# Kernel tuning notes

Measured on AMD Instinct MI355X. Metric: run time of the kernel, lower is better.

The kernel has to match this reference:

```python
import jax, jax.numpy as jnp
import numpy as np

N_TX = 1_000_000   # transaction nodes
N_W  = 250_000     # wallet nodes
E    = 2_000_000   # edges per relation
F_TX, F_W = 64, 32 # raw feature dims
H, OUT = 64, 2     # hidden, out (module defaults)


def setup_inputs() -> dict:
    key = jax.random.key(0)
    ks = jax.random.split(key, 40)
    f32 = jnp.float32
    def w(i, shape):
        return jax.random.normal(ks[i], shape, dtype=f32) * 0.05
    inp = {}
    inp["x_tx"] = jax.random.normal(ks[0], (N_TX, F_TX), dtype=f32)
    inp["x_w"]  = jax.random.normal(ks[1], (N_W, F_W), dtype=f32)
    inp["src_tw"] = jax.random.randint(ks[2], (E,), 0, N_TX)
    inp["dst_tw"] = jax.random.randint(ks[3], (E,), 0, N_W)
    inp["src_wt"] = jax.random.randint(ks[4], (E,), 0, N_W)
    inp["dst_wt"] = jax.random.randint(ks[5], (E,), 0, N_TX)
    # lin_in per node type
    inp["Win_tx"], inp["bin_tx"] = w(6, (F_TX, H)), w(7, (H,))
    inp["Win_w"],  inp["bin_w"]  = w(8, (F_W, H)),  w(9, (H,))
    # conv1: SAGEConv per edge type (lin_l has bias, lin_r no bias)
    inp["Wl1_tw"], inp["bl1_tw"], inp["Wr1_tw"] = w(10, (H, H)), w(11, (H,)), w(12, (H, H))
    inp["Wl1_wt"], inp["bl1_wt"], inp["Wr1_wt"] = w(13, (H, H)), w(14, (H,)), w(15, (H, H))
    # conv2
    inp["Wl2_tw"], inp["bl2_tw"], inp["Wr2_tw"] = w(16, (H, H)), w(17, (H,)), w(18, (H, H))
    inp["Wl2_wt"], inp["bl2_wt"], inp["Wr2_wt"] = w(19, (H, H)), w(20, (H,)), w(21, (H, H))
    # tx head
    inp["Wh1"], inp["bh1"] = w(22, (H, H)), w(23, (H,))
    inp["Wh2"], inp["bh2"] = w(24, (H, OUT)), w(25, (OUT,))
    return inp


def _sage(x_src, x_dst, src, dst, Wl, bl, Wr, n_dst):
    # PyG SAGEConv: lin_l(mean_{j->i} x_src[j]) + lin_r(x_dst[i])
    agg = jax.ops.segment_sum(x_src[src], dst, num_segments=n_dst)
    cnt = jax.ops.segment_sum(jnp.ones((src.shape[0],), x_src.dtype), dst,
                              num_segments=n_dst)
    mean = agg / jnp.maximum(cnt, 1.0)[:, None]
    return mean @ Wl + bl + x_dst @ Wr


def reference(x_tx, x_w, src_tw, dst_tw, src_wt, dst_wt,
              Win_tx, bin_tx, Win_w, bin_w,
              Wl1_tw, bl1_tw, Wr1_tw, Wl1_wt, bl1_wt, Wr1_wt,
              Wl2_tw, bl2_tw, Wr2_tw, Wl2_wt, bl2_wt, Wr2_wt,
              Wh1, bh1, Wh2, bh2):
    # per-type input projection
    h_tx = x_tx @ Win_tx + bin_tx   # [N_TX, H]
    h_w  = x_w @ Win_w + bin_w      # [N_W, H]
    # conv1 (HeteroConv aggr='sum'; each dst type has one relation) + relu
    w1 = jax.nn.relu(_sage(h_tx, h_w,  src_tw, dst_tw, Wl1_tw, bl1_tw, Wr1_tw, N_W))
    t1 = jax.nn.relu(_sage(h_w,  h_tx, src_wt, dst_wt, Wl1_wt, bl1_wt, Wr1_wt, N_TX))
    # conv2 + relu
    w2 = jax.nn.relu(_sage(t1, w1, src_tw, dst_tw, Wl2_tw, bl2_tw, Wr2_tw, N_W))
    t2 = jax.nn.relu(_sage(w1, t1, src_wt, dst_wt, Wl2_wt, bl2_wt, Wr2_wt, N_TX))
    # tx head (dropout inactive in eval)
    logits = jax.nn.relu(t2 @ Wh1 + bh1) @ Wh2 + bh2  # [N_TX, 2]
    return (logits, t2, w2)
```

## Files before the change

### kernel.cpp

```cpp
#include <hip/hip_runtime.h>
#include <hip/hip_bf16.h>

typedef __hip_bfloat16 bf16;
typedef __attribute__((ext_vector_type(8))) short bf16x8;
typedef __attribute__((ext_vector_type(4))) float f32x4;

__device__ __forceinline__ float b2f(bf16 v) { return __bfloat162float(v); }
__device__ __forceinline__ bf16 f2b(float v) { return __float2bfloat16(v); }
__device__ __forceinline__ unsigned short f2bb(float v) {
    unsigned int u = __float_as_uint(v);
    u += 0x7fffu + ((u >> 16) & 1u);
    return (unsigned short)(u >> 16);
}
__device__ __forceinline__ float b2fx(bf16x8 v, int k) {
    return __uint_as_float(((unsigned int)(unsigned short)v[k]) << 16);
}

__device__ __forceinline__ f32x4 mfma16(bf16x8 a, bf16x8 b, f32x4 c) {
    return __builtin_amdgcn_mfma_f32_16x16x32_bf16(a, b, c, 0, 0, 0);
}

__device__ __forceinline__ bf16x8 load_bfrag(const float* __restrict__ W, int k0, int col) {
    bf16x8 f;
#pragma unroll
    for (int j = 0; j < 8; ++j)
        f[j] = (short)f2bb(W[(size_t)(k0 + j) * 64 + col]);
    return f;
}

__device__ __forceinline__ int swzH(int row, int b) {
    return row * 128 + (b ^ ((row & 7) << 4));
}

__global__ void count_rank2_kernel(const int* __restrict__ dst_tw, int* __restrict__ deg_w,
                                   int* __restrict__ rank_tw, int ne_tw,
                                   const int* __restrict__ dst_wt, int* __restrict__ deg_tx,
                                   int* __restrict__ rank_wt, int ne_wt) {
    int e = blockIdx.x * 256 + threadIdx.x;
    if (e < ne_tw) rank_tw[e] = atomicAdd(&deg_w[dst_tw[e]], 1);
    else {
        int e2 = e - ne_tw;
        if (e2 < ne_wt) rank_wt[e2] = atomicAdd(&deg_tx[dst_wt[e2]], 1);
    }
}

__global__ void scan1m_kernel(const int* __restrict__ dw, int* __restrict__ ew,
                              int* __restrict__ pw, int nw, int npw,
                              const int* __restrict__ dt, int* __restrict__ et,
                              int* __restrict__ pt, int nt) {
    __shared__ int sT[256];
    const int* deg; int* excl; int* partial; int n; int b;
    if ((int)blockIdx.x < npw) { deg = dw; excl = ew; partial = pw; n = nw; b = blockIdx.x; }
    else { deg = dt; excl = et; partial = pt; n = nt; b = blockIdx.x - npw; }
    int tid = threadIdx.x;
    int base = b * 1024 + tid * 4;
    int v0 = (base + 0 < n) ? deg[base + 0] : 0;
    int v1 = (base + 1 < n) ? deg[base + 1] : 0;
    int v2 = (base + 2 < n) ? deg[base + 2] : 0;
    int v3 = (base + 3 < n) ? deg[base + 3] : 0;
    int t = v0 + v1 + v2 + v3;
    sT[tid] = t;
    __syncthreads();
    for (int off = 1; off < 256; off <<= 1) {
        int x = (tid >= off) ? sT[tid - off] : 0;
        __syncthreads();
        sT[tid] += x;
        __syncthreads();
    }
    int et2 = sT[tid] - t;
    if (tid == 255) partial[b] = sT[255];
    if (base + 0 < n) excl[base + 0] = et2;
    if (base + 1 < n) excl[base + 1] = et2 + v0;
    if (base + 2 < n) excl[base + 2] = et2 + v0 + v1;
    if (base + 3 < n) excl[base + 3] = et2 + v0 + v1 + v2;
}

__global__ void scan2m_kernel(int* __restrict__ pw, int npw, int* __restrict__ pt, int npt) {
    __shared__ int sT[256];
    __shared__ int carry;
    int* partial = blockIdx.x ? pt : pw;
    int np = blockIdx.x ? npt : npw;
    int tid = threadIdx.x;
    if (tid == 0) carry = 0;
    __syncthreads();
    for (int c = 0; c < np; c += 256) {
        int i = c + tid;
        int v = (i < np) ? partial[i] : 0;
        sT[tid] = v;
        __syncthreads();
        for (int off = 1; off < 256; off <<= 1) {
            int x = (tid >= off) ? sT[tid - off] : 0;
            __syncthreads();
            sT[tid] += x;
            __syncthreads();
        }
        int incl = sT[tid];
        int total = sT[255];
        if (i < np) partial[i] = carry + incl - v;
        __syncthreads();
        if (tid == 0) carry += total;
        __syncthreads();
    }
}

__global__ void scan3m_kernel(const int* __restrict__ ew, const int* __restrict__ pw,
                              int* __restrict__ rw, int nw, int nbw,
                              const int* __restrict__ et, const int* __restrict__ pt,
                              int* __restrict__ rt, int nt) {
    int b = blockIdx.x;
    const int* excl; const int* partial; int* rp; int n; int i;
    if (b < nbw) { i = b * 256 + threadIdx.x; excl = ew; partial = pw; rp = rw; n = nw; }
    else { i = (b - nbw) * 256 + threadIdx.x; excl = et; partial = pt; rp = rt; n = nt; }
    if (i < n) rp[i] = excl[i] + partial[i >> 10];
}

__device__ __forceinline__ void proj64_body(const float* __restrict__ x,
                                            const float* __restrict__ W,
                                            const float* __restrict__ b,
                                            bf16* __restrict__ out, int n, int bid) {
    int tid = threadIdx.x;
    int lane = tid & 63, w = tid >> 6;
    int lm = lane & 15, lq = lane >> 4;

    bf16x8 wc[4][2];
    float bv[4];
#pragma unroll
    for (int ct = 0; ct < 4; ++ct) {
        int colc = ct * 16 + lm;
        wc[ct][0] = load_bfrag(W, lq * 8, colc);
        wc[ct][1] = load_bfrag(W, 32 + lq * 8, colc);
        bv[ct] = b[colc];
    }

    int larow = w * 16 + lm;
    int row0 = bid * 512;
    if (row0 >= n) return;
    int ar = row0 + larow; ar = (ar < n) ? ar : (n - 1);
    const float* xrow = x + ((size_t)ar << 6);
    float4 p0 = *(const float4*)(xrow + lq * 8);
    float4 p1 = *(const float4*)(xrow + lq * 8 + 4);
    float4 p2 = *(const float4*)(xrow + 32 + lq * 8);
    float4 p3 = *(const float4*)(xrow + 32 + lq * 8 + 4);

    for (int g = 0; g < 8; ++g) {
        int gr0 = row0 + g * 64;
        if (gr0 >= n) break;
        float4 q0 = p0, q1 = p1, q2 = p2, q3 = p3;
        if (g < 7) {
            int nr = gr0 + 64 + larow; nr = (nr < n) ? nr : (n - 1);
            const float* nx = x + ((size_t)nr << 6);
            q0 = *(const float4*)(nx + lq * 8);
            q1 = *(const float4*)(nx + lq * 8 + 4);
            q2 = *(const float4*)(nx + 32 + lq * 8);
            q3 = *(const float4*)(nx + 32 + lq * 8 + 4);
        }
        bf16x8 a0, a1;
        a0[0] = (short)f2bb(p0.x); a0[1] = (short)f2bb(p0.y);
        a0[2] = (short)f2bb(p0.z); a0[3] = (short)f2bb(p0.w);
        a0[4] = (short)f2bb(p1.x); a0[5] = (short)f2bb(p1.y);
        a0[6] = (short)f2bb(p1.z); a0[7] = (short)f2bb(p1.w);
        a1[0] = (short)f2bb(p2.x); a1[1] = (short)f2bb(p2.y);
        a1[2] = (short)f2bb(p2.z); a1[3] = (short)f2bb(p2.w);
        a1[4] = (short)f2bb(p3.x); a1[5] = (short)f2bb(p3.y);
        a1[6] = (short)f2bb(p3.z); a1[7] = (short)f2bb(p3.w);
#pragma unroll
        for (int ct = 0; ct < 4; ++ct) {
            f32x4 acc = {0.f, 0.f, 0.f, 0.f};
            acc = mfma16(a0, wc[ct][0], acc);
            acc = mfma16(a1, wc[ct][1], acc);
            int colc = ct * 16 + lm;
#pragma unroll
            for (int r = 0; r < 4; ++r) {
                int grow = gr0 + w * 16 + lq * 4 + r;
                if (grow < n)
                    out[(size_t)grow * 64 + colc] = f2b(acc[r] + bv[ct]);
            }
        }
        p0 = q0; p1 = q1; p2 = q2; p3 = q3;
    }
}

__device__ __forceinline__ void proj32_body(const float* __restrict__ x,
                                            const float* __restrict__ W,
                                            const float* __restrict__ b,
                                            bf16* __restrict__ out, int n, int bid,
                                            float (*sW)[64], float* sb, float (*sx)[32]) {
    const int F = 32;
    int tid = threadIdx.x;
    for (int idx = tid; idx < F * 16; idx += 256)
        ((float4*)sW)[idx] = ((const float4*)W)[idx];
    if (tid < 64) sb[tid] = b[tid];
    int base = bid * 64;
    int w = tid >> 6, j = tid & 63;
    int lw = w * 4;
    for (int g = 0; g < 4; ++g) {
        int row0 = base + g * 16;
        __syncthreads();
        for (int idx = tid; idx < 4 * F; idx += 256) {
            int rr = idx / (F / 4), c4 = idx - rr * (F / 4);
            int row = row0 + rr;
            float4 v = (row < n) ? ((const float4*)x)[(size_t)row * (F / 4) + c4]
                                 : make_float4(0.f, 0.f, 0.f, 0.f);
            *(float4*)&sx[rr][c4 * 4] = v;
        }
        __syncthreads();
        float a0 = sb[j], a1 = sb[j], a2 = sb[j], a3 = sb[j];
#pragma unroll 2
        for (int k = 0; k < F; k += 4) {
            float w0 = sW[k][j], w1 = sW[k + 1][j], w2 = sW[k + 2][j], w3 = sW[k + 3][j];
            float4 m0 = *(const float4*)&sx[lw + 0][k];
            float4 m1 = *(const float4*)&sx[lw + 1][k];
            float4 m2 = *(const float4*)&sx[lw + 2][k];
            float4 m3 = *(const float4*)&sx[lw + 3][k];
            a0 += m0.x * w0 + m0.y * w1 + m0.z * w2 + m0.w * w3;
            a1 += m1.x * w0 + m1.y * w1 + m1.z * w2 + m1.w * w3;
            a2 += m2.x * w0 + m2.y * w1 + m2.z * w2 + m2.w * w3;
            a3 += m3.x * w0 + m3.y * w1 + m3.z * w2 + m3.w * w3;
        }
        int r0 = row0 + lw;
        if (r0 + 0 < n) out[(size_t)(r0 + 0) * 64 + j] = f2b(a0);
        if (r0 + 1 < n) out[(size_t)(r0 + 1) * 64 + j] = f2b(a1);
        if (r0 + 2 < n) out[(size_t)(r0 + 2) * 64 + j] = f2b(a2);
        if (r0 + 3 < n) out[(size_t)(r0 + 3) * 64 + j] = f2b(a3);
    }
}

__global__ __launch_bounds__(256)
void fused_front_kernel(const int* __restrict__ src_tw, const int* __restrict__ dst_tw,
                        const int* __restrict__ rank_tw, const int* __restrict__ rp_w,
                        int* __restrict__ col_tw, int ne_tw,
                        const int* __restrict__ src_wt, const int* __restrict__ dst_wt,
                        const int* __restrict__ rank_wt, const int* __restrict__ rp_tx,
                        int* __restrict__ col_wt, int ne_wt, int gsc,
                        const float* __restrict__ x_tx, const float* __restrict__ Win_tx,
                        const float* __restrict__ bin_tx, bf16* __restrict__ A, int n_tx, int gp64,
                        const float* __restrict__ x_w, const float* __restrict__ Win_w,
                        const float* __restrict__ bin_w, bf16* __restrict__ B, int n_w) {
    __shared__ float sW32[32][64];
    __shared__ float sb32[64];
    __shared__ float sx32[16][32];
    int bid = blockIdx.x;
    if (bid < gsc) {
        int e = bid * 256 + threadIdx.x;
        if (e < ne_tw) {
            col_tw[rp_w[dst_tw[e]] + rank_tw[e]] = src_tw[e];
        } else {
            int e2 = e - ne_tw;
            if (e2 < ne_wt)
                col_wt[rp_tx[dst_wt[e2]] + rank_wt[e2]] = src_wt[e2];
        }
    } else if (bid < gsc + gp64) {
        proj64_body(x_tx, Win_tx, bin_tx, A, n_tx, bid - gsc);
    } else {
        proj32_body(x_w, Win_w, bin_w, B, n_w, bid - gsc - gp64, sW32, sb32, sx32);
    }
}

#define GM_ACC(x, w) \
    a0 += (w) * b2fx(x, 0); a1 += (w) * b2fx(x, 1); \
    a2 += (w) * b2fx(x, 2); a3 += (w) * b2fx(x, 3); \
    a4 += (w) * b2fx(x, 4); a5 += (w) * b2fx(x, 5); \
    a6 += (w) * b2fx(x, 6); a7 += (w) * b2fx(x, 7);

__device__ __forceinline__ void gather_body(const bf16* __restrict__ h,
                                            const int* __restrict__ rowptr,
                                            const int* __restrict__ deg,
                                            const int* __restrict__ col,
                                            bf16* __restrict__ mean, int n, int bid) {
    int tid = threadIdx.x;
    int row = bid * 32 + (tid >> 3);
    if (row >= n) return;
    int fg = tid & 7;
    int base = rowptr[row];
    int d = deg[row];
    int lasto = (d > 0) ? d - 1 : 0;
    float a0 = 0.f, a1 = 0.f, a2 = 0.f, a3 = 0.f;
    float a4 = 0.f, a5 = 0.f, a6 = 0.f, a7 = 0.f;
    for (int e0 = 0; e0 < d; e0 += 8) {
        int o1 = (e0 + 1 < d) ? e0 + 1 : lasto;
        int o2 = (e0 + 2 < d) ? e0 + 2 : lasto;
        int o3 = (e0 + 3 < d) ? e0 + 3 : lasto;
        int o4 = (e0 + 4 < d) ? e0 + 4 : lasto;
        int o5 = (e0 + 5 < d) ? e0 + 5 : lasto;
        int o6 = (e0 + 6 < d) ? e0 + 6 : lasto;
        int o7 = (e0 + 7 < d) ? e0 + 7 : lasto;
        int s0 = col[base + e0], s1 = col[base + o1];
        int s2 = col[base + o2], s3 = col[base + o3];
        int s4 = col[base + o4], s5 = col[base + o5];
        int s6 = col[base + o6], s7 = col[base + o7];
        bf16x8 x0 = *(const bf16x8*)(h + ((size_t)s0 << 6) + (fg << 3));
        bf16x8 x1 = *(const bf16x8*)(h + ((size_t)s1 << 6) + (fg << 3));
        bf16x8 x2 = *(const bf16x8*)(h + ((size_t)s2 << 6) + (fg << 3));
        bf16x8 x3 = *(const bf16x8*)(h + ((size_t)s3 << 6) + (fg << 3));
        bf16x8 x4 = *(const bf16x8*)(h + ((size_t)s4 << 6) + (fg << 3));
        bf16x8 x5 = *(const bf16x8*)(h + ((size_t)s5 << 6) + (fg << 3));
        bf16x8 x6 = *(const bf16x8*)(h + ((size_t)s6 << 6) + (fg << 3));
        bf16x8 x7 = *(const bf16x8*)(h + ((size_t)s7 << 6) + (fg << 3));
        float w1 = (e0 + 1 < d) ? 1.f : 0.f;
        float w2 = (e0 + 2 < d) ? 1.f : 0.f;
        float w3 = (e0 + 3 < d) ? 1.f : 0.f;
        float w4 = (e0 + 4 < d) ? 1.f : 0.f;
        float w5 = (e0 + 5 < d) ? 1.f : 0.f;
        float w6 = (e0 + 6 < d) ? 1.f : 0.f;
        float w7 = (e0 + 7 < d) ? 1.f : 0.f;
        GM_ACC(x0, 1.f)
        GM_ACC(x1, w1)
        GM_ACC(x2, w2)
        GM_ACC(x3, w3)
        GM_ACC(x4, w4)
        GM_ACC(x5, w5)
        GM_ACC(x6, w6)
        GM_ACC(x7, w7)
    }
    float dd = fmaxf((float)d, 1.f);
    bf16x8 o;
    o[0] = (short)f2bb(a0 / dd); o[1] = (short)f2bb(a1 / dd);
    o[2] = (short)f2bb(a2 / dd); o[3] = (short)f2bb(a3 / dd);
    o[4] = (short)f2bb(a4 / dd); o[5] = (short)f2bb(a5 / dd);
    o[6] = (short)f2bb(a6 / dd); o[7] = (short)f2bb(a7 / dd);
    *(bf16x8*)(mean + ((size_t)row << 6) + (fg << 3)) = o;
}

__global__ __launch_bounds__(256)
void gather2_kernel(const bf16* __restrict__ hw, const int* __restrict__ rpw,
                    const int* __restrict__ dw, const int* __restrict__ cw,
                    bf16* __restrict__ mw, int nw, int gbw,
                    const bf16* __restrict__ ht, const int* __restrict__ rpt,
                    const int* __restrict__ dt, const int* __restrict__ ct,
                    bf16* __restrict__ mt, int nt) {
    if ((int)blockIdx.x < gbw) gather_body(hw, rpw, dw, cw, mw, nw, blockIdx.x);
    else                       gather_body(ht, rpt, dt, ct, mt, nt, blockIdx.x - gbw);
}

template<bool HEAD>
__device__ __forceinline__ void sage_body(
        const bf16* __restrict__ mean, const bf16* __restrict__ xd,
        const float* __restrict__ Wl, const float* __restrict__ bl,
        const float* __restrict__ Wr,
        float* __restrict__ outf, bf16* __restrict__ outb,
        const float* __restrict__ Wh1, const float* __restrict__ bh1,
        const float* __restrict__ Wh2, const float* __restrict__ bh2,
        float* __restrict__ logits, int n, int bid, short* sH) {
    int tid = threadIdx.x;
    int lane = tid & 63, w = tid >> 6;
    int lm = lane & 15, lq = lane >> 4;

    bf16x8 wc[4][4];
    bf16x8 wh[4][2];
    float blv[4], h1v[4], w2a[4], w2b[4];
#pragma unroll
    for (int ct = 0; ct < 4; ++ct) {
        int colc = ct * 16 + lm;
        wc[ct][0] = load_bfrag(Wl, lq * 8, colc);
        wc[ct][1] = load_bfrag(Wl, 32 + lq * 8, colc);
        wc[ct][2] = load_bfrag(Wr, lq * 8, colc);
        wc[ct][3] = load_bfrag(Wr, 32 + lq * 8, colc);
        blv[ct] = bl[colc];
        if (HEAD) {
            wh[ct][0] = load_bfrag(Wh1, lq * 8, colc);
            wh[ct][1] = load_bfrag(Wh1, 32 + lq * 8, colc);
            h1v[ct] = bh1[colc];
            w2a[ct] = Wh2[colc * 2 + 0];
            w2b[ct] = Wh2[colc * 2 + 1];
        }
    }
    float b20 = 0.f, b21 = 0.f;
    if (HEAD) { b20 = bh2[0]; b21 = bh2[1]; }

    int larow = w * 16 + lm;
    int row0 = bid * 512;
    if (row0 >= n) return;
    int ar = row0 + larow; ar = (ar < n) ? ar : (n - 1);
    const bf16* mrow = mean + ((size_t)ar << 6);
    const bf16* xrow = xd + ((size_t)ar << 6);
    bf16x8 a0 = *(const bf16x8*)(mrow + lq * 8);
    bf16x8 a1 = *(const bf16x8*)(mrow + 32 + lq * 8);
    bf16x8 a2 = *(const bf16x8*)(xrow + lq * 8);
    bf16x8 a3 = *(const bf16x8*)(xrow + 32 + lq * 8);

    for (int g = 0; g < 8; ++g) {
        int gr0 = row0 + g * 64;
        if (gr0 >= n) break;
        bf16x8 n0 = a0, n1 = a1, n2 = a2, n3 = a3;
        if (g < 7) {
            int nr = gr0 + 64 + larow; nr = (nr < n) ? nr : (n - 1);
            const bf16* nm = mean + ((size_t)nr << 6);
            const bf16* nx = xd + ((size_t)nr << 6);
            n0 = *(const bf16x8*)(nm + lq * 8);
            n1 = *(const bf16x8*)(nm + 32 + lq * 8);
            n2 = *(const bf16x8*)(nx + lq * 8);
            n3 = *(const bf16x8*)(nx + 32 + lq * 8);
        }
#pragma unroll
        for (int ct = 0; ct < 4; ++ct) {
            f32x4 acc = {0.f, 0.f, 0.f, 0.f};
            acc = mfma16(a0, wc[ct][0], acc);
            acc = mfma16(a1, wc[ct][1], acc);
            acc = mfma16(a2, wc[ct][2], acc);
            acc = mfma16(a3, wc[ct][3], acc);
            int colc = ct * 16 + lm;
#pragma unroll
            for (int r = 0; r < 4; ++r) {
                int lrow = w * 16 + lq * 4 + r;
                int grow = gr0 + lrow;
                float v = fmaxf(acc[r] + blv[ct], 0.f);
                if (grow < n) {
                    if (outf) outf[(size_t)grow * 64 + colc] = v;
                    if (outb) outb[(size_t)grow * 64 + colc] = f2b(v);
                }
                if (HEAD)
                    *(short*)((char*)sH + swzH(lrow, colc * 2)) = (short)f2bb(v);
            }
        }
        if (HEAD) {
            bf16x8 h0 = *(const bf16x8*)((char*)sH + swzH(larow, lq * 16));
            bf16x8 h1 = *(const bf16x8*)((char*)sH + swzH(larow, 64 + lq * 16));
            float qa0 = 0.f, qa1 = 0.f, qa2 = 0.f, qa3 = 0.f;
            float qb0 = 0.f, qb1 = 0.f, qb2 = 0.f, qb3 = 0.f;
#pragma unroll
            for (int ct = 0; ct < 4; ++ct) {
                f32x4 acc = {0.f, 0.f, 0.f, 0.f};
                acc = mfma16(h0, wh[ct][0], acc);
                acc = mfma16(h1, wh[ct][1], acc);
                float hb = h1v[ct];
                float h_0 = fmaxf(acc[0] + hb, 0.f);
                float h_1 = fmaxf(acc[1] + hb, 0.f);
                float h_2 = fmaxf(acc[2] + hb, 0.f);
                float h_3 = fmaxf(acc[3] + hb, 0.f);
                qa0 += h_0 * w2a[ct]; qb0 += h_0 * w2b[ct];
                qa1 += h_1 * w2a[ct]; qb1 += h_1 * w2b[ct];
                qa2 += h_2 * w2a[ct]; qb2 += h_2 * w2b[ct];
                qa3 += h_3 * w2a[ct]; qb3 += h_3 * w2b[ct];
            }
#pragma unroll
            for (int m = 8; m; m >>= 1) {
                qa0 += __shfl_xor(qa0, m); qb0 += __shfl_xor(qb0, m);
                qa1 += __shfl_xor(qa1, m); qb1 += __shfl_xor(qb1, m);
                qa2 += __shfl_xor(qa2, m); qb2 += __shfl_xor(qb2, m);
                qa3 += __shfl_xor(qa3, m); qb3 += __shfl_xor(qb3, m);
            }
            int rowb = gr0 + w * 16 + lq * 4;
            if (lm == 0) {
                if (rowb + 0 < n) { logits[(size_t)(rowb + 0) * 2 + 0] = qa0 + b20;
                                    logits[(size_t)(rowb + 0) * 2 + 1] = qb0 + b21; }
                if (rowb + 1 < n) { logits[(size_t)(rowb + 1) * 2 + 0] = qa1 + b20;
                                    logits[(size_t)(rowb + 1) * 2 + 1] = qb1 + b21; }
                if (rowb + 2 < n) { logits[(size_t)(rowb + 2) * 2 + 0] = qa2 + b20;
                                    logits[(size_t)(rowb + 2) * 2 + 1] = qb2 + b21; }
                if (rowb + 3 < n) { logits[(size_t)(rowb + 3) * 2 + 0] = qa3 + b20;
                                    logits[(size_t)(rowb + 3) * 2 + 1] = qb3 + b21; }
            }
        }
        a0 = n0; a1 = n1; a2 = n2; a3 = n3;
    }
}

template<bool HEAD>
__global__ __launch_bounds__(256, 2)
void sage2_kernel(const bf16* __restrict__ mw, const bf16* __restrict__ xw,
                  const float* __restrict__ Wlw, const float* __restrict__ blw,
                  const float* __restrict__ Wrw,
                  float* __restrict__ outfw, bf16* __restrict__ outbw, int nw, int gbw,
                  const bf16* __restrict__ mt, const bf16* __restrict__ xt,
                  const float* __restrict__ Wlt, const float* __restrict__ blt,
                  const float* __restrict__ Wrt,
                  float* __restrict__ outft, bf16* __restrict__ outbt,
                  const float* __restrict__ Wh1, const float* __restrict__ bh1,
                  const float* __restrict__ Wh2, const float* __restrict__ bh2,
                  float* __restrict__ logits, int nt) {
    __shared__ __align__(16) short sH[HEAD ? 64 * 64 : 8];
    if ((int)blockIdx.x < gbw)
        sage_body<false>(mw, xw, Wlw, blw, Wrw, outfw, outbw,
                         nullptr, nullptr, nullptr, nullptr, nullptr, nw, blockIdx.x, sH);
    else
        sage_body<HEAD>(mt, xt, Wlt, blt, Wrt, outft, outbt,
                        Wh1, bh1, Wh2, bh2, logits, nt, blockIdx.x - gbw, sH);
}

extern "C" void kernel_launch(void* const* d_in, const int* in_sizes, int n_in,
                              void* d_out, int out_size, void* d_ws, size_t ws_size,
                              hipStream_t stream) {
    const float* x_tx   = (const float*)d_in[0];
    const float* x_w    = (const float*)d_in[1];
    const int*   src_tw = (const int*)d_in[2];
    const int*   dst_tw = (const int*)d_in[3];
    const int*   src_wt = (const int*)d_in[4];
    const int*   dst_wt = (const int*)d_in[5];
    const float* Win_tx = (const float*)d_in[6];
    const float* bin_tx = (const float*)d_in[7];
    const float* Win_w  = (const float*)d_in[8];
    const float* bin_w  = (const float*)d_in[9];
    const float* Wl1_tw = (const float*)d_in[10];
    const float* bl1_tw = (const float*)d_in[11];
    const float* Wr1_tw = (const float*)d_in[12];
    const float* Wl1_wt = (const float*)d_in[13];
    const float* bl1_wt = (const float*)d_in[14];
    const float* Wr1_wt = (const float*)d_in[15];
    const float* Wl2_tw = (const float*)d_in[16];
    const float* bl2_tw = (const float*)d_in[17];
    const float* Wr2_tw = (const float*)d_in[18];
    const float* Wl2_wt = (const float*)d_in[19];
    const float* bl2_wt = (const float*)d_in[20];
    const float* Wr2_wt = (const float*)d_in[21];
    const float* Wh1    = (const float*)d_in[22];
    const float* bh1    = (const float*)d_in[23];
    const float* Wh2    = (const float*)d_in[24];
    const float* bh2    = (const float*)d_in[25];

    const int n_tx  = in_sizes[0] / 64;
    const int n_w   = in_sizes[1] / 32;
    const int ne_tw = in_sizes[2];
    const int ne_wt = in_sizes[4];

    bf16* mean_tx = (bf16*)d_ws;
    bf16* mean_w  = mean_tx + (size_t)n_tx * 64;
    bf16* A       = mean_w + (size_t)n_w * 64;
    bf16* B       = A + (size_t)n_tx * 64;
    int*  deg_w   = (int*)(B + (size_t)n_w * 64);
    int*  deg_tx  = deg_w + n_w;
    int*  rp_w    = deg_tx + n_tx;
    int*  rp_tx   = rp_w + n_w;
    int*  ex_w    = rp_tx + n_tx;
    int*  ex_tx   = ex_w + n_w;
    int*  col_tw  = ex_tx + n_tx;
    int*  col_wt  = col_tw + ne_tw;
    int*  rank_tw = col_wt + ne_wt;
    int*  rank_wt = rank_tw + ne_tw;
    int*  part_w  = rank_wt + ne_wt;
    int*  part_tx = part_w + 4096;

    float* out_logits = (float*)d_out;
    float* out_t2 = out_logits + (size_t)n_tx * 2;
    float* out_w2 = out_t2 + (size_t)n_tx * 64;

    dim3 blk(256);
    int gp64 = (n_tx + 511) / 512;
    int gp32 = (n_w + 63) / 64;
    int gs_w  = (n_w + 511) / 512;
    int gs_tx = (n_tx + 511) / 512;
    int gg_w  = (n_w + 31) / 32;
    int gg_tx = (n_tx + 31) / 32;
    int gsc = (ne_tw + ne_wt + 255) / 256;
    int np_w  = (n_w + 1023) / 1024;
    int np_tx = (n_tx + 1023) / 1024;
    int nbw = (n_w + 255) / 256;
    int nbt = (n_tx + 255) / 256;

    hipMemsetAsync(deg_w, 0, (size_t)n_w * sizeof(int), stream);
    hipMemsetAsync(deg_tx, 0, (size_t)n_tx * sizeof(int), stream);
    count_rank2_kernel<<<gsc, blk, 0, stream>>>(dst_tw, deg_w, rank_tw, ne_tw,
                                                dst_wt, deg_tx, rank_wt, ne_wt);
    scan1m_kernel<<<np_w + np_tx, blk, 0, stream>>>(deg_w, ex_w, part_w, n_w, np_w,
                                                    deg_tx, ex_tx, part_tx, n_tx);
    scan2m_kernel<<<2, blk, 0, stream>>>(part_w, np_w, part_tx, np_tx);
    scan3m_kernel<<<nbw + nbt, blk, 0, stream>>>(ex_w, part_w, rp_w, n_w, nbw,
                                                 ex_tx, part_tx, rp_tx, n_tx);

    fused_front_kernel<<<gsc + gp64 + gp32, blk, 0, stream>>>(
        src_tw, dst_tw, rank_tw, rp_w, col_tw, ne_tw,
        src_wt, dst_wt, rank_wt, rp_tx, col_wt, ne_wt, gsc,
        x_tx, Win_tx, bin_tx, A, n_tx, gp64,
        x_w, Win_w, bin_w, B, n_w);

    gather2_kernel<<<gg_w + gg_tx, blk, 0, stream>>>(
        A, rp_w, deg_w, col_tw, mean_w, n_w, gg_w,
        B, rp_tx, deg_tx, col_wt, mean_tx, n_tx);
    sage2_kernel<false><<<gs_w + gs_tx, blk, 0, stream>>>(
        mean_w, B, Wl1_tw, bl1_tw, Wr1_tw, nullptr, B, n_w, gs_w,
        mean_tx, A, Wl1_wt, bl1_wt, Wr1_wt, nullptr, A,
        nullptr, nullptr, nullptr, nullptr, nullptr, n_tx);

    gather2_kernel<<<gg_w + gg_tx, blk, 0, stream>>>(
        A, rp_w, deg_w, col_tw, mean_w, n_w, gg_w,
        B, rp_tx, deg_tx, col_wt, mean_tx, n_tx);
    sage2_kernel<true><<<gs_w + gs_tx, blk, 0, stream>>>(
        mean_w, B, Wl2_tw, bl2_tw, Wr2_tw, out_w2, nullptr, n_w, gs_w,
        mean_tx, A, Wl2_wt, bl2_wt, Wr2_wt, out_t2, nullptr,
        Wh1, bh1, Wh2, bh2, out_logits, n_tx);
}
```

Before: 1.370 ms.

## Fuse neighbor mean-gather into SAGE MFMA kernel, removing mean buffers

Each SAGE layer now does its CSR neighbor gather inside the MFMA kernel. Every lane accumulates the mean directly into its A-fragment registers, so the separate gather kernel and the mean_w/mean_tx round trip through global memory go away. Because the fused kernel reads the previous layer's output while writing new outputs, it adds ping-pong buffers A2/B2 instead of updating in place. The cost is a different gather parallelism: per row, 4 lanes each load two 16-byte chunks with 4-edge unrolling, replacing 8 lanes per row with 8-edge unrolling. The next-row prefetch is dropped and the occupancy hint in launch_bounds is removed, so latency hiding during the gather may suffer.

```diff
diff --git a/kernel.cpp b/kernel.cpp
--- a/kernel.cpp
+++ b/kernel.cpp
@@ -256,85 +256,22 @@
     }
 }
 
-#define GM_ACC(x, w) \
-    a0 += (w) * b2fx(x, 0); a1 += (w) * b2fx(x, 1); \
-    a2 += (w) * b2fx(x, 2); a3 += (w) * b2fx(x, 3); \
-    a4 += (w) * b2fx(x, 4); a5 += (w) * b2fx(x, 5); \
-    a6 += (w) * b2fx(x, 6); a7 += (w) * b2fx(x, 7);
-
-__device__ __forceinline__ void gather_body(const bf16* __restrict__ h,
-                                            const int* __restrict__ rowptr,
-                                            const int* __restrict__ deg,
-                                            const int* __restrict__ col,
-                                            bf16* __restrict__ mean, int n, int bid) {
-    int tid = threadIdx.x;
-    int row = bid * 32 + (tid >> 3);
-    if (row >= n) return;
-    int fg = tid & 7;
-    int base = rowptr[row];
-    int d = deg[row];
-    int lasto = (d > 0) ? d - 1 : 0;
-    float a0 = 0.f, a1 = 0.f, a2 = 0.f, a3 = 0.f;
-    float a4 = 0.f, a5 = 0.f, a6 = 0.f, a7 = 0.f;
-    for (int e0 = 0; e0 < d; e0 += 8) {
-        int o1 = (e0 + 1 < d) ? e0 + 1 : lasto;
-        int o2 = (e0 + 2 < d) ? e0 + 2 : lasto;
-        int o3 = (e0 + 3 < d) ? e0 + 3 : lasto;
-        int o4 = (e0 + 4 < d) ? e0 + 4 : lasto;
-        int o5 = (e0 + 5 < d) ? e0 + 5 : lasto;
-        int o6 = (e0 + 6 < d) ? e0 + 6 : lasto;
-        int o7 = (e0 + 7 < d) ? e0 + 7 : lasto;
-        int s0 = col[base + e0], s1 = col[base + o1];
-        int s2 = col[base + o2], s3 = col[base + o3];
-        int s4 = col[base + o4], s5 = col[base + o5];
-        int s6 = col[base + o6], s7 = col[base + o7];
-        bf16x8 x0 = *(const bf16x8*)(h + ((size_t)s0 << 6) + (fg << 3));
-        bf16x8 x1 = *(const bf16x8*)(h + ((size_t)s1 << 6) + (fg << 3));
-        bf16x8 x2 = *(const bf16x8*)(h + ((size_t)s2 << 6) + (fg << 3));
-        bf16x8 x3 = *(const bf16x8*)(h + ((size_t)s3 << 6) + (fg << 3));
-        bf16x8 x4 = *(const bf16x8*)(h + ((size_t)s4 << 6) + (fg << 3));
-        bf16x8 x5 = *(const bf16x8*)(h + ((size_t)s5 << 6) + (fg << 3));
-        bf16x8 x6 = *(const bf16x8*)(h + ((size_t)s6 << 6) + (fg << 3));
-        bf16x8 x7 = *(const bf16x8*)(h + ((size_t)s7 << 6) + (fg << 3));
-        float w1 = (e0 + 1 < d) ? 1.f : 0.f;
-        float w2 = (e0 + 2 < d) ? 1.f : 0.f;
-        float w3 = (e0 + 3 < d) ? 1.f : 0.f;
-        float w4 = (e0 + 4 < d) ? 1.f : 0.f;
-        float w5 = (e0 + 5 < d) ? 1.f : 0.f;
-        float w6 = (e0 + 6 < d) ? 1.f : 0.f;
-        float w7 = (e0 + 7 < d) ? 1.f : 0.f;
-        GM_ACC(x0, 1.f)
-        GM_ACC(x1, w1)
-        GM_ACC(x2, w2)
-        GM_ACC(x3, w3)
-        GM_ACC(x4, w4)
-        GM_ACC(x5, w5)
-        GM_ACC(x6, w6)
-        GM_ACC(x7, w7)
-    }
-    float dd = fmaxf((float)d, 1.f);
-    bf16x8 o;
-    o[0] = (short)f2bb(a0 / dd); o[1] = (short)f2bb(a1 / dd);
-    o[2] = (short)f2bb(a2 / dd); o[3] = (short)f2bb(a3 / dd);
-    o[4] = (short)f2bb(a4 / dd); o[5] = (short)f2bb(a5 / dd);
-    o[6] = (short)f2bb(a6 / dd); o[7] = (short)f2bb(a7 / dd);
-    *(bf16x8*)(mean + ((size_t)row << 6) + (fg << 3)) = o;
-}
-
-__global__ __launch_bounds__(256)
-void gather2_kernel(const bf16* __restrict__ hw, const int* __restrict__ rpw,
-                    const int* __restrict__ dw, const int* __restrict__ cw,
-                    bf16* __restrict__ mw, int nw, int gbw,
-                    const bf16* __restrict__ ht, const int* __restrict__ rpt,
-                    const int* __restrict__ dt, const int* __restrict__ ct,
-                    bf16* __restrict__ mt, int nt) {
-    if ((int)blockIdx.x < gbw) gather_body(hw, rpw, dw, cw, mw, nw, blockIdx.x);
-    else                       gather_body(ht, rpt, dt, ct, mt, nt, blockIdx.x - gbw);
-}
+#define GA4(x, wt) \
+    p0 += (wt) * b2fx(x, 0); p1 += (wt) * b2fx(x, 1); \
+    p2 += (wt) * b2fx(x, 2); p3 += (wt) * b2fx(x, 3); \
+    p4 += (wt) * b2fx(x, 4); p5 += (wt) * b2fx(x, 5); \
+    p6 += (wt) * b2fx(x, 6); p7 += (wt) * b2fx(x, 7);
+#define GB4(x, wt) \
+    q0 += (wt) * b2fx(x, 0); q1 += (wt) * b2fx(x, 1); \
+    q2 += (wt) * b2fx(x, 2); q3 += (wt) * b2fx(x, 3); \
+    q4 += (wt) * b2fx(x, 4); q5 += (wt) * b2fx(x, 5); \
+    q6 += (wt) * b2fx(x, 6); q7 += (wt) * b2fx(x, 7);
 
 template<bool HEAD>
-__device__ __forceinline__ void sage_body(
-        const bf16* __restrict__ mean, const bf16* __restrict__ xd,
+__device__ __forceinline__ void sageg_body(
+        const bf16* __restrict__ hsrc, const int* __restrict__ rowptr,
+        const int* __restrict__ deg, const int* __restrict__ col,
+        const bf16* __restrict__ xd,
         const float* __restrict__ Wl, const float* __restrict__ bl,
         const float* __restrict__ Wr,
         float* __restrict__ outf, bf16* __restrict__ outb,
@@ -370,27 +307,60 @@
     int larow = w * 16 + lm;
     int row0 = bid * 512;
     if (row0 >= n) return;
-    int ar = row0 + larow; ar = (ar < n) ? ar : (n - 1);
-    const bf16* mrow = mean + ((size_t)ar << 6);
-    const bf16* xrow = xd + ((size_t)ar << 6);
-    bf16x8 a0 = *(const bf16x8*)(mrow + lq * 8);
-    bf16x8 a1 = *(const bf16x8*)(mrow + 32 + lq * 8);
-    bf16x8 a2 = *(const bf16x8*)(xrow + lq * 8);
-    bf16x8 a3 = *(const bf16x8*)(xrow + 32 + lq * 8);
+    int fo1 = lq * 8, fo2 = 32 + lq * 8;
 
     for (int g = 0; g < 8; ++g) {
         int gr0 = row0 + g * 64;
         if (gr0 >= n) break;
-        bf16x8 n0 = a0, n1 = a1, n2 = a2, n3 = a3;
-        if (g < 7) {
-            int nr = gr0 + 64 + larow; nr = (nr < n) ? nr : (n - 1);
-            const bf16* nm = mean + ((size_t)nr << 6);
-            const bf16* nx = xd + ((size_t)nr << 6);
-            n0 = *(const bf16x8*)(nm + lq * 8);
-            n1 = *(const bf16x8*)(nm + 32 + lq * 8);
-            n2 = *(const bf16x8*)(nx + lq * 8);
-            n3 = *(const bf16x8*)(nx + 32 + lq * 8);
-        }
+        int arow = gr0 + larow;
+        int ar = (arow < n) ? arow : (n - 1);
+        const bf16* xrow = xd + ((size_t)ar << 6);
+        bf16x8 a2 = *(const bf16x8*)(xrow + fo1);
+        bf16x8 a3 = *(const bf16x8*)(xrow + fo2);
+        int base = rowptr[ar];
+        int d = deg[ar];
+        int lasto = (d > 0) ? d - 1 : 0;
+        float p0 = 0.f, p1 = 0.f, p2 = 0.f, p3 = 0.f;
+        float p4 = 0.f, p5 = 0.f, p6 = 0.f, p7 = 0.f;
+        float q0 = 0.f, q1 = 0.f, q2 = 0.f, q3 = 0.f;
+        float q4 = 0.f, q5 = 0.f, q6 = 0.f, q7 = 0.f;
+        for (int e0 = 0; e0 < d; e0 += 4) {
+            int o1 = (e0 + 1 < d) ? e0 + 1 : lasto;
+            int o2 = (e0 + 2 < d) ? e0 + 2 : lasto;
+            int o3 = (e0 + 3 < d) ? e0 + 3 : lasto;
+            int s0 = col[base + e0], s1 = col[base + o1];
+            int s2 = col[base + o2], s3 = col[base + o3];
+            const bf16* r0p = hsrc + ((size_t)s0 << 6);
+            const bf16* r1p = hsrc + ((size_t)s1 << 6);
+            const bf16* r2p = hsrc + ((size_t)s2 << 6);
+            const bf16* r3p = hsrc + ((size_t)s3 << 6);
+            bf16x8 xa0 = *(const bf16x8*)(r0p + fo1);
+            bf16x8 xb0 = *(const bf16x8*)(r0p + fo2);
+            bf16x8 xa1 = *(const bf16x8*)(r1p + fo1);
+            bf16x8 xb1 = *(const bf16x8*)(r1p + fo2);
+            bf16x8 xa2 = *(const bf16x8*)(r2p + fo1);
+            bf16x8 xb2 = *(const bf16x8*)(r2p + fo2);
+            bf16x8 xa3 = *(const bf16x8*)(r3p + fo1);
+            bf16x8 xb3 = *(const bf16x8*)(r3p + fo2);
+            float w1 = (e0 + 1 < d) ? 1.f : 0.f;
+            float w2 = (e0 + 2 < d) ? 1.f : 0.f;
+            float w3 = (e0 + 3 < d) ? 1.f : 0.f;
+            GA4(xa0, 1.f) GB4(xb0, 1.f)
+            GA4(xa1, w1)  GB4(xb1, w1)
+            GA4(xa2, w2)  GB4(xb2, w2)
+            GA4(xa3, w3)  GB4(xb3, w3)
+        }
+        float dd = fmaxf((float)d, 1.f);
+        bf16x8 a0, a1;
+        a0[0] = (short)f2bb(p0 / dd); a0[1] = (short)f2bb(p1 / dd);
+        a0[2] = (short)f2bb(p2 / dd); a0[3] = (short)f2bb(p3 / dd);
+        a0[4] = (short)f2bb(p4 / dd); a0[5] = (short)f2bb(p5 / dd);
+        a0[6] = (short)f2bb(p6 / dd); a0[7] = (short)f2bb(p7 / dd);
+        a1[0] = (short)f2bb(q0 / dd); a1[1] = (short)f2bb(q1 / dd);
+        a1[2] = (short)f2bb(q2 / dd); a1[3] = (short)f2bb(q3 / dd);
+        a1[4] = (short)f2bb(q4 / dd); a1[5] = (short)f2bb(q5 / dd);
+        a1[6] = (short)f2bb(q6 / dd); a1[7] = (short)f2bb(q7 / dd);
+
 #pragma unroll
         for (int ct = 0; ct < 4; ++ct) {
             f32x4 acc = {0.f, 0.f, 0.f, 0.f};
@@ -451,30 +421,33 @@
                                     logits[(size_t)(rowb + 3) * 2 + 1] = qb3 + b21; }
             }
         }
-        a0 = n0; a1 = n1; a2 = n2; a3 = n3;
     }
 }
 
 template<bool HEAD>
-__global__ __launch_bounds__(256, 2)
-void sage2_kernel(const bf16* __restrict__ mw, const bf16* __restrict__ xw,
-                  const float* __restrict__ Wlw, const float* __restrict__ blw,
-                  const float* __restrict__ Wrw,
-                  float* __restrict__ outfw, bf16* __restrict__ outbw, int nw, int gbw,
-                  const bf16* __restrict__ mt, const bf16* __restrict__ xt,
-                  const float* __restrict__ Wlt, const float* __restrict__ blt,
-                  const float* __restrict__ Wrt,
-                  float* __restrict__ outft, bf16* __restrict__ outbt,
-                  const float* __restrict__ Wh1, const float* __restrict__ bh1,
-                  const float* __restrict__ Wh2, const float* __restrict__ bh2,
-                  float* __restrict__ logits, int nt) {
+__global__ __launch_bounds__(256)
+void sageg2_kernel(const bf16* __restrict__ hw, const int* __restrict__ rpw,
+                   const int* __restrict__ dgw, const int* __restrict__ clw,
+                   const bf16* __restrict__ xw,
+                   const float* __restrict__ Wlw, const float* __restrict__ blw,
+                   const float* __restrict__ Wrw,
+                   float* __restrict__ outfw, bf16* __restrict__ outbw, int nw, int gbw,
+                   const bf16* __restrict__ ht, const int* __restrict__ rpt,
+                   const int* __restrict__ dgt, const int* __restrict__ clt,
+                   const bf16* __restrict__ xt,
+                   const float* __restrict__ Wlt, const float* __restrict__ blt,
+                   const float* __restrict__ Wrt,
+                   float* __restrict__ outft, bf16* __restrict__ outbt,
+                   const float* __restrict__ Wh1, const float* __restrict__ bh1,
+                   const float* __restrict__ Wh2, const float* __restrict__ bh2,
+                   float* __restrict__ logits, int nt) {
     __shared__ __align__(16) short sH[HEAD ? 64 * 64 : 8];
     if ((int)blockIdx.x < gbw)
-        sage_body<false>(mw, xw, Wlw, blw, Wrw, outfw, outbw,
-                         nullptr, nullptr, nullptr, nullptr, nullptr, nw, blockIdx.x, sH);
+        sageg_body<false>(hw, rpw, dgw, clw, xw, Wlw, blw, Wrw, outfw, outbw,
+                          nullptr, nullptr, nullptr, nullptr, nullptr, nw, blockIdx.x, sH);
     else
-        sage_body<HEAD>(mt, xt, Wlt, blt, Wrt, outft, outbt,
-                        Wh1, bh1, Wh2, bh2, logits, nt, blockIdx.x - gbw, sH);
+        sageg_body<HEAD>(ht, rpt, dgt, clt, xt, Wlt, blt, Wrt, outft, outbt,
+                         Wh1, bh1, Wh2, bh2, logits, nt, blockIdx.x - gbw, sH);
 }
 
 extern "C" void kernel_launch(void* const* d_in, const int* in_sizes, int n_in,
@@ -512,9 +485,9 @@
     const int ne_tw = in_sizes[2];
     const int ne_wt = in_sizes[4];
 
-    bf16* mean_tx = (bf16*)d_ws;
-    bf16* mean_w  = mean_tx + (size_t)n_tx * 64;
-    bf16* A       = mean_w + (size_t)n_w * 64;
+    bf16* A2      = (bf16*)d_ws;
+    bf16* B2      = A2 + (size_t)n_tx * 64;
+    bf16* A       = B2 + (size_t)n_w * 64;
     bf16* B       = A + (size_t)n_tx * 64;
     int*  deg_w   = (int*)(B + (size_t)n_w * 64);
     int*  deg_tx  = deg_w + n_w;
@@ -538,8 +511,6 @@
     int gp32 = (n_w + 63) / 64;
     int gs_w  = (n_w + 511) / 512;
     int gs_tx = (n_tx + 511) / 512;
-    int gg_w  = (n_w + 31) / 32;
-    int gg_tx = (n_tx + 31) / 32;
     int gsc = (ne_tw + ne_wt + 255) / 256;
     int np_w  = (n_w + 1023) / 1024;
     int np_tx = (n_tx + 1023) / 1024;
@@ -562,19 +533,13 @@
         x_tx, Win_tx, bin_tx, A, n_tx, gp64,
         x_w, Win_w, bin_w, B, n_w);
 
-    gather2_kernel<<<gg_w + gg_tx, blk, 0, stream>>>(
-        A, rp_w, deg_w, col_tw, mean_w, n_w, gg_w,
-        B, rp_tx, deg_tx, col_wt, mean_tx, n_tx);
-    sage2_kernel<false><<<gs_w + gs_tx, blk, 0, stream>>>(
-        mean_w, B, Wl1_tw, bl1_tw, Wr1_tw, nullptr, B, n_w, gs_w,
-        mean_tx, A, Wl1_wt, bl1_wt, Wr1_wt, nullptr, A,
+    sageg2_kernel<false><<<gs_w + gs_tx, blk, 0, stream>>>(
+        A, rp_w, deg_w, col_tw, B, Wl1_tw, bl1_tw, Wr1_tw, nullptr, B2, n_w, gs_w,
+        B, rp_tx, deg_tx, col_wt, A, Wl1_wt, bl1_wt, Wr1_wt, nullptr, A2,
         nullptr, nullptr, nullptr, nullptr, nullptr, n_tx);
 
-    gather2_kernel<<<gg_w + gg_tx, blk, 0, stream>>>(
-        A, rp_w, deg_w, col_tw, mean_w, n_w, gg_w,
-        B, rp_tx, deg_tx, col_wt, mean_tx, n_tx);
-    sage2_kernel<true><<<gs_w + gs_tx, blk, 0, stream>>>(
-        mean_w, B, Wl2_tw, bl2_tw, Wr2_tw, out_w2, nullptr, n_w, gs_w,
-        mean_tx, A, Wl2_wt, bl2_wt, Wr2_wt, out_t2, nullptr,
+    sageg2_kernel<true><<<gs_w + gs_tx, blk, 0, stream>>>(
+        A2, rp_w, deg_w, col_tw, B2, Wl2_tw, bl2_tw, Wr2_tw, out_w2, nullptr, n_w, gs_w,
+        B2, rp_tx, deg_tx, col_wt, A2, Wl2_wt, bl2_wt, Wr2_wt, out_t2, nullptr,
         Wh1, bh1, Wh2, bh2, out_logits, n_tx);
 }
```

New measurement: 1.342 ms. -2.0%, faster.
